# Kernel tuning notes

Hardware: AMD Instinct MI355X
Metric: run time of the kernel (lower is better)

## Reference

```python
import jax, jax.numpy as jnp
import numpy as np

SIM_THRESHOLD = 0.95
NUM_SAMPLES = 2048
EPS_NORM = 1e-12  # F.normalize eps
EPS_DENOM = 1e-6


def setup_inputs() -> dict:
    key = jax.random.key(0)
    k1, k2, k3 = jax.random.split(key, 3)
    B, K, C, H, W = 2, 8, 256, 128, 128
    masks_logits = jax.random.normal(k1, (B, K, H, W), dtype=jnp.float32)
    upsampler_features = jax.random.normal(k2, (B, C, H, W), dtype=jnp.float32)
    # per-batch randperm[:S], mirroring torch.randperm(H*W)[:S]
    perm_keys = jax.random.split(k3, B)
    indices = jnp.stack([
        jax.random.permutation(pk, H * W)[:NUM_SAMPLES] for pk in perm_keys
    ]).astype(jnp.int32)  # (B, S)
    return {"masks_logits": masks_logits,
            "upsampler_features": upsampler_features,
            "indices": indices}


def reference(masks_logits, upsampler_features, indices):
    B, K, H, W = masks_logits.shape
    C = upsampler_features.shape[1]
    probs = jax.nn.sigmoid(masks_logits).reshape(B, K, H * W)
    feats = upsampler_features.reshape(B, C, H * W)
    idx = indices[:, None, :]  # (B,1,S)
    f_sample = jnp.take_along_axis(feats, idx, axis=2)          # (B,C,S)
    norm = jnp.linalg.norm(f_sample, axis=1, keepdims=True)
    f_sample = f_sample / jnp.maximum(norm, EPS_NORM)
    m_sample = jnp.take_along_axis(probs, idx, axis=2)          # (B,K,S)
    sim = jnp.einsum('bcs,bct->bst', f_sample, f_sample)        # (B,S,S)
    pos = (sim > SIM_THRESHOLD).astype(jnp.float32)             # (B,S,S)
    m_diff = jnp.abs(m_sample[:, :, :, None] - m_sample[:, :, None, :])  # (B,K,S,S)
    num = jnp.sum(m_diff * pos[:, None, :, :])
    den = jnp.sum(pos) + EPS_DENOM
    return num / den
```

## Files before the change

### kernel.cpp

```cpp
#include <hip/hip_runtime.h>
#include <hip/hip_bf16.h>
#include <math.h>

#define Bn 2
#define Kn 8
#define Cn 256
#define HWn (128*128)
#define Sn 2048
#define BT 128
#define BKc 128
#define NSTAGE (Cn / BKc)
#define SIM_BLOCKS ((Sn/BT)*(Sn/BT)*Bn)

typedef __bf16 bf16x8 __attribute__((ext_vector_type(8)));
typedef float  f32x4  __attribute__((ext_vector_type(4)));

__device__ __forceinline__ void gload_lds16(const ushort* g, ushort* l) {
    __builtin_amdgcn_global_load_lds(
        (const __attribute__((address_space(1))) void*)g,
        (__attribute__((address_space(3))) void*)l,
        16, 0, 0);
}

__device__ __forceinline__ float bf16_to_f32(ushort u) {
    union { unsigned int i; float f; } cv;
    cv.i = ((unsigned int)u) << 16;
    return cv.f;
}

__global__ __launch_bounds__(256) void transpose_kernel(
    const float* __restrict__ feats, ushort* __restrict__ featsT)
{
    __shared__ float lds[64][65];
    const int b  = blockIdx.z;
    const int C0 = blockIdx.y * 64;
    const int H0 = blockIdx.x * 64;
    const int t  = threadIdx.x;

    const float* base = feats + ((size_t)(b * Cn + C0)) * HWn + H0;
    const int c_l = t >> 4;
    const int h4  = (t & 15) * 4;
    #pragma unroll
    for (int i = 0; i < 4; ++i) {
        const float4 v = *reinterpret_cast<const float4*>(
            base + (size_t)(c_l + 16 * i) * HWn + h4);
        lds[h4 + 0][c_l + 16 * i] = v.x;
        lds[h4 + 1][c_l + 16 * i] = v.y;
        lds[h4 + 2][c_l + 16 * i] = v.z;
        lds[h4 + 3][c_l + 16 * i] = v.w;
    }
    __syncthreads();
    const int h  = t >> 2;
    const int c0 = (t & 3) * 16;
    ushort u[16];
    #pragma unroll
    for (int e = 0; e < 16; ++e) {
        __hip_bfloat16 hv = __float2bfloat16(lds[h][c0 + e]);
        u[e] = *reinterpret_cast<const ushort*>(&hv);
    }
    ushort* dst = featsT + ((size_t)(b * HWn + H0 + h)) * Cn + C0 + c0;
    *reinterpret_cast<uint4*>(dst)     = *reinterpret_cast<const uint4*>(&u[0]);
    *reinterpret_cast<uint4*>(dst + 8) = *reinterpret_cast<const uint4*>(&u[8]);
}

__global__ __launch_bounds__(256) void gather2_kernel(
    const float* __restrict__ masks, const ushort* __restrict__ featsT,
    const int* __restrict__ indices, ushort* __restrict__ fTb,
    float* __restrict__ mS)
{
    const int wave = threadIdx.x >> 6;
    const int lane = threadIdx.x & 63;
    const int bs = blockIdx.x * 4 + wave;
    const int b  = bs >> 11;
    const int s  = bs & (Sn - 1);
    const int id = indices[b * Sn + s];

    const ushort4 raw = *reinterpret_cast<const ushort4*>(
        featsT + ((size_t)(b * HWn + id)) * Cn + lane * 4);
    float v[4] = { bf16_to_f32(raw.x), bf16_to_f32(raw.y),
                   bf16_to_f32(raw.z), bf16_to_f32(raw.w) };

    float x = v[0]*v[0] + v[1]*v[1] + v[2]*v[2] + v[3]*v[3];
    #pragma unroll
    for (int o = 32; o > 0; o >>= 1) x += __shfl_xor(x, o);
    const float scale = 1.0f / fmaxf(sqrtf(x), 1e-12f);

    ushort o4[4];
    #pragma unroll
    for (int q = 0; q < 4; ++q) {
        __hip_bfloat16 hv = __float2bfloat16(v[q] * scale);
        o4[q] = *reinterpret_cast<const ushort*>(&hv);
    }
    *reinterpret_cast<ushort4*>(fTb + (size_t)bs * Cn + lane * 4) =
        *reinterpret_cast<const ushort4*>(&o4[0]);

    if (lane < Kn) {
        const float lg = masks[((size_t)(b * Kn + lane)) * HWn + id];
        mS[(size_t)bs * Kn + lane] = 1.0f / (1.0f + expf(-lg));
    }
}

__global__ __launch_bounds__(256) void gather_kernel(
    const float* __restrict__ masks, const float* __restrict__ feats,
    const int* __restrict__ indices, ushort* __restrict__ fTb,
    float* __restrict__ mS)
{
    const int wave = threadIdx.x >> 6;
    const int lane = threadIdx.x & 63;
    const int bs = blockIdx.x * 4 + wave;
    const int b  = bs >> 11;
    const int s  = bs & (Sn - 1);
    const int id = indices[b * Sn + s];

    const float* fb = feats + (size_t)b * Cn * HWn + id;
    float v[4];
    #pragma unroll
    for (int q = 0; q < 4; ++q)
        v[q] = fb[(size_t)(lane + 64 * q) * HWn];

    float x = v[0]*v[0] + v[1]*v[1] + v[2]*v[2] + v[3]*v[3];
    #pragma unroll
    for (int o = 32; o > 0; o >>= 1) x += __shfl_xor(x, o);
    const float scale = 1.0f / fmaxf(sqrtf(x), 1e-12f);

    #pragma unroll
    for (int q = 0; q < 4; ++q) {
        __hip_bfloat16 hv = __float2bfloat16(v[q] * scale);
        fTb[(size_t)bs * Cn + lane + 64 * q] = *reinterpret_cast<const ushort*>(&hv);
    }

    if (lane < Kn) {
        const float lg = masks[((size_t)(b * Kn + lane)) * HWn + id];
        mS[(size_t)bs * Kn + lane] = 1.0f / (1.0f + expf(-lg));
    }
}

__global__ __launch_bounds__(512, 4) void sim_kernel(
    const ushort* __restrict__ fTb, const float* __restrict__ mS,
    float* __restrict__ part)
{
    __shared__ ushort ldsA[BT * BKc];
    __shared__ ushort ldsB[BT * BKc];

    const int b   = blockIdx.z;
    const int s0  = blockIdx.y * BT;
    const int t0  = blockIdx.x * BT;
    const int tid = threadIdx.x;
    const int lane = tid & 63;
    const int wave = tid >> 6;
    const int wm = wave >> 2;
    const int wn = wave & 3;
    const int l15 = lane & 15, l4 = lane >> 4;

    const ushort* FA = fTb + ((size_t)(b * Sn + s0)) * Cn;
    const ushort* FB = fTb + ((size_t)(b * Sn + t0)) * Cn;

    f32x4 acc[4][2];
    #pragma unroll
    for (int m = 0; m < 4; ++m)
        #pragma unroll
        for (int n = 0; n < 2; ++n) acc[m][n] = (f32x4){0.f, 0.f, 0.f, 0.f};

    #pragma unroll
    for (int st = 0; st < NSTAGE; ++st) {
        const int k0 = st * BKc;
        #pragma unroll
        for (int i = 0; i < 4; ++i) {
            const int q   = tid + i * 512;
            const int row = q >> 4;
            const int csw = (q & 15) ^ (row & 15);
            const size_t goff = (size_t)row * Cn + k0 + csw * 8;
            gload_lds16(FA + goff, &ldsA[q * 8]);
            gload_lds16(FB + goff, &ldsB[q * 8]);
        }
        __syncthreads();

        #pragma unroll
        for (int kk = 0; kk < BKc; kk += 32) {
            const int g = (kk >> 3) + l4;
            bf16x8 aF[4], bF[2];
            #pragma unroll
            for (int m = 0; m < 4; ++m) {
                const int row = wm * 64 + m * 16 + l15;
                aF[m] = *reinterpret_cast<const bf16x8*>(
                    &ldsA[row * BKc + ((g ^ (row & 15)) << 3)]);
            }
            #pragma unroll
            for (int n = 0; n < 2; ++n) {
                const int row = wn * 32 + n * 16 + l15;
                bF[n] = *reinterpret_cast<const bf16x8*>(
                    &ldsB[row * BKc + ((g ^ (row & 15)) << 3)]);
            }
            #pragma unroll
            for (int m = 0; m < 4; ++m)
                #pragma unroll
                for (int n = 0; n < 2; ++n)
                    acc[m][n] = __builtin_amdgcn_mfma_f32_16x16x32_bf16(
                        aF[m], bF[n], acc[m][n], 0, 0, 0);
        }
        __syncthreads();
    }

    float num_l = 0.0f, den_l = 0.0f;
    const float* mSb = mS + (size_t)b * Sn * Kn;
    #pragma unroll
    for (int m = 0; m < 4; ++m) {
        #pragma unroll
        for (int n = 0; n < 2; ++n) {
            #pragma unroll
            for (int r = 0; r < 4; ++r) {
                if (acc[m][n][r] > 0.95f) {
                    den_l += 1.0f;
                    const int srow = s0 + wm * 64 + m * 16 + l4 * 4 + r;
                    const int tcol = t0 + wn * 32 + n * 16 + l15;
                    const float* ma = mSb + (size_t)srow * Kn;
                    const float* mb = mSb + (size_t)tcol * Kn;
                    #pragma unroll
                    for (int k = 0; k < Kn; ++k) num_l += fabsf(ma[k] - mb[k]);
                }
            }
        }
    }

    #pragma unroll
    for (int o = 32; o > 0; o >>= 1) {
        num_l += __shfl_down(num_l, o);
        den_l += __shfl_down(den_l, o);
    }
    __shared__ float rn[8], rd[8];
    if (lane == 0) { rn[wave] = num_l; rd[wave] = den_l; }
    __syncthreads();
    if (tid == 0) {
        float nn = 0.f, dd = 0.f;
        #pragma unroll
        for (int w = 0; w < 8; ++w) { nn += rn[w]; dd += rd[w]; }
        const int bid = (blockIdx.z * gridDim.y + blockIdx.y) * gridDim.x + blockIdx.x;
        part[2 * bid]     = nn;
        part[2 * bid + 1] = dd;
    }
}

__global__ __launch_bounds__(256) void finalize_kernel(
    const float* __restrict__ part, float* __restrict__ out)
{
    const int tid = threadIdx.x;
    float n = 0.f, d = 0.f;
    #pragma unroll
    for (int i = 0; i < SIM_BLOCKS / 256; ++i) {
        const float2 p = reinterpret_cast<const float2*>(part)[tid + 256 * i];
        n += p.x; d += p.y;
    }
    #pragma unroll
    for (int o = 32; o > 0; o >>= 1) {
        n += __shfl_down(n, o);
        d += __shfl_down(d, o);
    }
    __shared__ float sn[4], sd[4];
    if ((tid & 63) == 0) { sn[tid >> 6] = n; sd[tid >> 6] = d; }
    __syncthreads();
    if (tid == 0) {
        const float fn = sn[0] + sn[1] + sn[2] + sn[3];
        const float fd = sd[0] + sd[1] + sd[2] + sd[3];
        out[0] = fn / (fd + 1e-6f);
    }
}

extern "C" void kernel_launch(void* const* d_in, const int* in_sizes, int n_in,
                              void* d_out, int out_size, void* d_ws, size_t ws_size,
                              hipStream_t stream) {
    const float* masks   = (const float*)d_in[0];
    const float* feats   = (const float*)d_in[1];
    const int*   indices = (const int*)d_in[2];
    float* out = (float*)d_out;

    const size_t fTb_b   = (size_t)Bn * Sn * Cn * sizeof(ushort);
    const size_t mS_b    = (size_t)Bn * Sn * Kn * sizeof(float);
    const size_t part_b  = (size_t)SIM_BLOCKS * 2 * sizeof(float);
    const size_t featsT_b = (size_t)Bn * HWn * Cn * sizeof(ushort);

    ushort* fTb   = (ushort*)d_ws;
    float*  mSm   = (float*)((char*)d_ws + fTb_b);
    float*  part  = (float*)((char*)d_ws + fTb_b + mS_b);
    ushort* featsT = (ushort*)((char*)d_ws + fTb_b + mS_b + part_b);

    if (ws_size >= fTb_b + mS_b + part_b + featsT_b) {
        dim3 tg(HWn / 64, Cn / 64, Bn);
        transpose_kernel<<<tg, 256, 0, stream>>>(feats, featsT);
        gather2_kernel<<<Bn * Sn / 4, 256, 0, stream>>>(masks, featsT, indices, fTb, mSm);
    } else {
        gather_kernel<<<Bn * Sn / 4, 256, 0, stream>>>(masks, feats, indices, fTb, mSm);
    }
    dim3 grid(Sn / BT, Sn / BT, Bn);
    sim_kernel<<<grid, 512, 0, stream>>>(fTb, mSm, part);
    finalize_kernel<<<1, 256, 0, stream>>>(part, out);
}
```

Baseline: 28.15 us.

## Fuse transpose into gather and compute only upper-triangular similarity tiles

The separate transpose and gather kernels are replaced by one kernel. It streams each 64-column slab of features into LDS as bf16, builds an inverse index map for that slab, and then normalizes and writes only the sampled columns. This removes the full bf16 transposed-feature buffer write and its later reread. The similarity kernel now launches only upper-triangular tile pairs and counts pairs with srow < tcol. The finalize step doubles the sums and adds the diagonal count analytically, roughly halving the MFMA and epilogue work. This relies on the indices being unique and on self-similarity always exceeding the threshold after bf16 rounding.

Measured after the change: 27.82 us. About the same (-1.2%).

```diff
diff --git a/kernel.cpp b/kernel.cpp
--- a/kernel.cpp
+++ b/kernel.cpp
@@ -10,7 +10,10 @@
 #define BT 128
 #define BKc 128
 #define NSTAGE (Cn / BKc)
-#define SIM_BLOCKS ((Sn/BT)*(Sn/BT)*Bn)
+#define NT (Sn / BT)
+#define NTRI (NT*(NT+1)/2)
+#define NPART (NTRI * Bn)
+#define TLH 64
 
 typedef __bf16 bf16x8 __attribute__((ext_vector_type(8)));
 typedef float  f32x4  __attribute__((ext_vector_type(4)));
@@ -27,111 +30,68 @@
     cv.i = ((unsigned int)u) << 16;
     return cv.f;
 }
-
-__global__ __launch_bounds__(256) void transpose_kernel(
-    const float* __restrict__ feats, ushort* __restrict__ featsT)
-{
-    __shared__ float lds[64][65];
-    const int b  = blockIdx.z;
-    const int C0 = blockIdx.y * 64;
-    const int H0 = blockIdx.x * 64;
-    const int t  = threadIdx.x;
-
-    const float* base = feats + ((size_t)(b * Cn + C0)) * HWn + H0;
-    const int c_l = t >> 4;
-    const int h4  = (t & 15) * 4;
-    #pragma unroll
-    for (int i = 0; i < 4; ++i) {
-        const float4 v = *reinterpret_cast<const float4*>(
-            base + (size_t)(c_l + 16 * i) * HWn + h4);
-        lds[h4 + 0][c_l + 16 * i] = v.x;
-        lds[h4 + 1][c_l + 16 * i] = v.y;
-        lds[h4 + 2][c_l + 16 * i] = v.z;
-        lds[h4 + 3][c_l + 16 * i] = v.w;
-    }
-    __syncthreads();
-    const int h  = t >> 2;
-    const int c0 = (t & 3) * 16;
-    ushort u[16];
-    #pragma unroll
-    for (int e = 0; e < 16; ++e) {
-        __hip_bfloat16 hv = __float2bfloat16(lds[h][c0 + e]);
-        u[e] = *reinterpret_cast<const ushort*>(&hv);
-    }
-    ushort* dst = featsT + ((size_t)(b * HWn + H0 + h)) * Cn + C0 + c0;
-    *reinterpret_cast<uint4*>(dst)     = *reinterpret_cast<const uint4*>(&u[0]);
-    *reinterpret_cast<uint4*>(dst + 8) = *reinterpret_cast<const uint4*>(&u[8]);
-}
-
-__global__ __launch_bounds__(256) void gather2_kernel(
-    const float* __restrict__ masks, const ushort* __restrict__ featsT,
-    const int* __restrict__ indices, ushort* __restrict__ fTb,
-    float* __restrict__ mS)
-{
-    const int wave = threadIdx.x >> 6;
-    const int lane = threadIdx.x & 63;
-    const int bs = blockIdx.x * 4 + wave;
-    const int b  = bs >> 11;
-    const int s  = bs & (Sn - 1);
-    const int id = indices[b * Sn + s];
-
-    const ushort4 raw = *reinterpret_cast<const ushort4*>(
-        featsT + ((size_t)(b * HWn + id)) * Cn + lane * 4);
-    float v[4] = { bf16_to_f32(raw.x), bf16_to_f32(raw.y),
-                   bf16_to_f32(raw.z), bf16_to_f32(raw.w) };
-
-    float x = v[0]*v[0] + v[1]*v[1] + v[2]*v[2] + v[3]*v[3];
-    #pragma unroll
-    for (int o = 32; o > 0; o >>= 1) x += __shfl_xor(x, o);
-    const float scale = 1.0f / fmaxf(sqrtf(x), 1e-12f);
-
-    ushort o4[4];
-    #pragma unroll
-    for (int q = 0; q < 4; ++q) {
-        __hip_bfloat16 hv = __float2bfloat16(v[q] * scale);
-        o4[q] = *reinterpret_cast<const ushort*>(&hv);
-    }
-    *reinterpret_cast<ushort4*>(fTb + (size_t)bs * Cn + lane * 4) =
-        *reinterpret_cast<const ushort4*>(&o4[0]);
-
-    if (lane < Kn) {
-        const float lg = masks[((size_t)(b * Kn + lane)) * HWn + id];
-        mS[(size_t)bs * Kn + lane] = 1.0f / (1.0f + expf(-lg));
-    }
-}
-
-__global__ __launch_bounds__(256) void gather_kernel(
+__device__ __forceinline__ ushort f32_to_bf16u(float f) {
+    __hip_bfloat16 hv = __float2bfloat16(f);
+    return *reinterpret_cast<const ushort*>(&hv);
+}
+
+__global__ __launch_bounds__(256) void gatherT_kernel(
     const float* __restrict__ masks, const float* __restrict__ feats,
     const int* __restrict__ indices, ushort* __restrict__ fTb,
     float* __restrict__ mS)
 {
-    const int wave = threadIdx.x >> 6;
-    const int lane = threadIdx.x & 63;
-    const int bs = blockIdx.x * 4 + wave;
-    const int b  = bs >> 11;
-    const int s  = bs & (Sn - 1);
-    const int id = indices[b * Sn + s];
-
-    const float* fb = feats + (size_t)b * Cn * HWn + id;
-    float v[4];
-    #pragma unroll
-    for (int q = 0; q < 4; ++q)
-        v[q] = fb[(size_t)(lane + 64 * q) * HWn];
-
-    float x = v[0]*v[0] + v[1]*v[1] + v[2]*v[2] + v[3]*v[3];
-    #pragma unroll
-    for (int o = 32; o > 0; o >>= 1) x += __shfl_xor(x, o);
-    const float scale = 1.0f / fmaxf(sqrtf(x), 1e-12f);
-
-    #pragma unroll
-    for (int q = 0; q < 4; ++q) {
-        __hip_bfloat16 hv = __float2bfloat16(v[q] * scale);
-        fTb[(size_t)bs * Cn + lane + 64 * q] = *reinterpret_cast<const ushort*>(&hv);
-    }
-
-    if (lane < Kn) {
-        const float lg = masks[((size_t)(b * Kn + lane)) * HWn + id];
-        mS[(size_t)bs * Kn + lane] = 1.0f / (1.0f + expf(-lg));
+    __shared__ ushort tile[Cn][TLH + 4];
+    __shared__ int smap[TLH];
+
+    const int b  = blockIdx.y;
+    const int h0 = blockIdx.x * TLH;
+    const int t  = threadIdx.x;
+    const int lane = t & 63;
+    const int wave = t >> 6;
+
+    if (t < TLH) smap[t] = -1;
+    __syncthreads();
+
+    #pragma unroll
+    for (int i = 0; i < 8; ++i) {
+        const int s  = t * 8 + i;
+        const int d  = indices[b * Sn + s] - h0;
+        if ((unsigned)d < TLH) smap[d] = s;
+    }
+
+    const float* fb = feats + ((size_t)b * Cn) * HWn + h0;
+    const int c_l = t >> 4;
+    const int h4  = (t & 15) * 4;
+    #pragma unroll
+    for (int it = 0; it < 16; ++it) {
+        const int c = c_l + 16 * it;
+        const float4 v = *reinterpret_cast<const float4*>(fb + (size_t)c * HWn + h4);
+        ushort4 u;
+        u.x = f32_to_bf16u(v.x); u.y = f32_to_bf16u(v.y);
+        u.z = f32_to_bf16u(v.z); u.w = f32_to_bf16u(v.w);
+        *reinterpret_cast<ushort4*>(&tile[c][h4]) = u;
+    }
+    __syncthreads();
+
+    for (int hs = wave; hs < TLH; hs += 4) {
+        const int p = smap[hs];
+        if (p < 0) continue;
+        float v[4];
+        #pragma unroll
+        for (int q = 0; q < 4; ++q)
+            v[q] = bf16_to_f32(tile[lane + 64 * q][hs]);
+        float x = v[0]*v[0] + v[1]*v[1] + v[2]*v[2] + v[3]*v[3];
+        #pragma unroll
+        for (int o = 32; o > 0; o >>= 1) x += __shfl_xor(x, o);
+        const float scale = 1.0f / fmaxf(sqrtf(x), 1e-12f);
+        #pragma unroll
+        for (int q = 0; q < 4; ++q)
+            fTb[(size_t)(b * Sn + p) * Cn + lane + 64 * q] =
+                f32_to_bf16u(v[q] * scale);
+        if (lane < Kn) {
+            const float lg = masks[((size_t)(b * Kn + lane)) * HWn + h0 + hs];
+            mS[(size_t)(b * Sn + p) * Kn + lane] = 1.0f / (1.0f + expf(-lg));
+        }
     }
 }
 
@@ -142,9 +102,13 @@
     __shared__ ushort ldsA[BT * BKc];
     __shared__ ushort ldsB[BT * BKc];
 
-    const int b   = blockIdx.z;
-    const int s0  = blockIdx.y * BT;
-    const int t0  = blockIdx.x * BT;
+    const int b = blockIdx.y;
+    int i = 0, rem = blockIdx.x;
+    while (rem >= NT - i) { rem -= NT - i; ++i; }
+    const int j  = i + rem;
+    const int s0 = i * BT;
+    const int t0 = j * BT;
+
     const int tid = threadIdx.x;
     const int lane = tid & 63;
     const int wave = tid >> 6;
@@ -165,8 +129,8 @@
     for (int st = 0; st < NSTAGE; ++st) {
         const int k0 = st * BKc;
         #pragma unroll
-        for (int i = 0; i < 4; ++i) {
-            const int q   = tid + i * 512;
+        for (int i2 = 0; i2 < 4; ++i2) {
+            const int q   = tid + i2 * 512;
             const int row = q >> 4;
             const int csw = (q & 15) ^ (row & 15);
             const size_t goff = (size_t)row * Cn + k0 + csw * 8;
@@ -209,10 +173,10 @@
         for (int n = 0; n < 2; ++n) {
             #pragma unroll
             for (int r = 0; r < 4; ++r) {
-                if (acc[m][n][r] > 0.95f) {
+                const int srow = s0 + wm * 64 + m * 16 + l4 * 4 + r;
+                const int tcol = t0 + wn * 32 + n * 16 + l15;
+                if (acc[m][n][r] > 0.95f && srow < tcol) {
                     den_l += 1.0f;
-                    const int srow = s0 + wm * 64 + m * 16 + l4 * 4 + r;
-                    const int tcol = t0 + wn * 32 + n * 16 + l15;
                     const float* ma = mSb + (size_t)srow * Kn;
                     const float* mb = mSb + (size_t)tcol * Kn;
                     #pragma unroll
@@ -234,7 +198,7 @@
         float nn = 0.f, dd = 0.f;
         #pragma unroll
         for (int w = 0; w < 8; ++w) { nn += rn[w]; dd += rd[w]; }
-        const int bid = (blockIdx.z * gridDim.y + blockIdx.y) * gridDim.x + blockIdx.x;
+        const int bid = blockIdx.y * NTRI + blockIdx.x;
         part[2 * bid]     = nn;
         part[2 * bid + 1] = dd;
     }
@@ -246,9 +210,12 @@
     const int tid = threadIdx.x;
     float n = 0.f, d = 0.f;
     #pragma unroll
-    for (int i = 0; i < SIM_BLOCKS / 256; ++i) {
-        const float2 p = reinterpret_cast<const float2*>(part)[tid + 256 * i];
-        n += p.x; d += p.y;
+    for (int i = 0; i < 2; ++i) {
+        const int idx = tid + 256 * i;
+        if (idx < NPART) {
+            const float2 p = reinterpret_cast<const float2*>(part)[idx];
+            n += p.x; d += p.y;
+        }
     }
     #pragma unroll
     for (int o = 32; o > 0; o >>= 1) {
@@ -259,8 +226,9 @@
     if ((tid & 63) == 0) { sn[tid >> 6] = n; sd[tid >> 6] = d; }
     __syncthreads();
     if (tid == 0) {
-        const float fn = sn[0] + sn[1] + sn[2] + sn[3];
-        const float fd = sd[0] + sd[1] + sd[2] + sd[3];
+        const float fn = 2.0f * (sn[0] + sn[1] + sn[2] + sn[3]);
+        const float fd = 2.0f * (sd[0] + sd[1] + sd[2] + sd[3])
+                       + (float)(Bn * Sn);
         out[0] = fn / (fd + 1e-6f);
     }
 }
@@ -273,24 +241,16 @@
     const int*   indices = (const int*)d_in[2];
     float* out = (float*)d_out;
 
-    const size_t fTb_b   = (size_t)Bn * Sn * Cn * sizeof(ushort);
-    const size_t mS_b    = (size_t)Bn * Sn * Kn * sizeof(float);
-    const size_t part_b  = (size_t)SIM_BLOCKS * 2 * sizeof(float);
-    const size_t featsT_b = (size_t)Bn * HWn * Cn * sizeof(ushort);
-
-    ushort* fTb   = (ushort*)d_ws;
-    float*  mSm   = (float*)((char*)d_ws + fTb_b);
-    float*  part  = (float*)((char*)d_ws + fTb_b + mS_b);
-    ushort* featsT = (ushort*)((char*)d_ws + fTb_b + mS_b + part_b);
-
-    if (ws_size >= fTb_b + mS_b + part_b + featsT_b) {
-        dim3 tg(HWn / 64, Cn / 64, Bn);
-        transpose_kernel<<<tg, 256, 0, stream>>>(feats, featsT);
-        gather2_kernel<<<Bn * Sn / 4, 256, 0, stream>>>(masks, featsT, indices, fTb, mSm);
-    } else {
-        gather_kernel<<<Bn * Sn / 4, 256, 0, stream>>>(masks, feats, indices, fTb, mSm);
-    }
-    dim3 grid(Sn / BT, Sn / BT, Bn);
+    const size_t fTb_b = (size_t)Bn * Sn * Cn * sizeof(ushort);
+    const size_t mS_b  = (size_t)Bn * Sn * Kn * sizeof(float);
+
+    ushort* fTb  = (ushort*)d_ws;
+    float*  mSm  = (float*)((char*)d_ws + fTb_b);
+    float*  part = (float*)((char*)d_ws + fTb_b + mS_b);
+
+    dim3 gg(HWn / TLH, Bn);
+    gatherT_kernel<<<gg, 256, 0, stream>>>(masks, feats, indices, fTb, mSm);
+    dim3 grid(NTRI, Bn);
     sim_kernel<<<grid, 512, 0, stream>>>(fTb, mSm, part);
     finalize_kernel<<<1, 256, 0, stream>>>(part, out);
 }
```
